# Kernel tuning notes

Measured on AMD Instinct MI355X. Metric: run time of the kernel, lower is better.

## Reference

```python
import jax, jax.numpy as jnp
import numpy as np

D_MODEL = 1024
SEL_DIM = 64
CONFIGS = [(4, 32), (8, 64), (16, 128)]  # (heads, dim)
B, T = 2, 2048


def setup_inputs() -> dict:
    key = jax.random.key(0)
    ks = jax.random.split(key, 20)
    s = 0.02  # init scale for stability
    inp = {
        "x": jax.random.normal(ks[0], (B, T, D_MODEL), jnp.float32),
        "sel_w1": jax.random.normal(ks[1], (SEL_DIM, D_MODEL), jnp.float32) * s,
        "sel_b1": jnp.zeros((SEL_DIM,), jnp.float32),
        "sel_w2": jax.random.normal(ks[2], (SEL_DIM, SEL_DIM), jnp.float32) * s,
        "sel_b2": jnp.zeros((SEL_DIM,), jnp.float32),
        "sel_w3": jax.random.normal(ks[3], (len(CONFIGS), SEL_DIM), jnp.float32) * s,
        "sel_b3": jnp.zeros((len(CONFIGS),), jnp.float32),
    }
    for i, (h, d) in enumerate(CONFIGS):
        inp[f"qw{i}"] = jax.random.normal(ks[4 + 3 * i], (h * d, D_MODEL), jnp.float32) * s
        inp[f"kw{i}"] = jax.random.normal(ks[5 + 3 * i], (d, D_MODEL), jnp.float32) * s
        inp[f"ww{i}"] = jax.random.normal(ks[6 + 3 * i], (h, D_MODEL), jnp.float32) * s
    return inp


def _seq_features(x):
    # x: [b,t,d]
    b, t, d = x.shape
    seq_mean = jnp.mean(x, axis=1, keepdims=True)            # [b,1,d]
    seq_std = jnp.std(x, axis=1, keepdims=True, ddof=1)      # torch.std is unbiased
    pos = (jnp.arange(t, dtype=x.dtype) / t)[None, :, None]  # [1,t,1] broadcast to [b,t,d]
    return x + seq_mean + seq_std + pos * 0.1


def _forward(x, sel_w1, sel_b1, sel_w2, sel_b2, sel_w3, sel_b3,
             qw0, kw0, ww0, qw1, kw1, ww1, qw2, kw2, ww2):
    b, t, dm = x.shape
    feats = _seq_features(x)
    h1 = jax.nn.relu(feats @ sel_w1.T + sel_b1)
    h2 = jax.nn.relu(h1 @ sel_w2.T + sel_b2)
    config_probs = jax.nn.softmax(h2 @ sel_w3.T + sel_b3, axis=-1)  # [b,t,ncfg]

    per_cfg = [(qw0, kw0, ww0), (qw1, kw1, ww1), (qw2, kw2, ww2)]
    final = jnp.zeros((b, t, t), dtype=x.dtype)
    for i, ((heads, dim), (qw, kw, ww)) in enumerate(zip(CONFIGS, per_cfg)):
        q = (x @ qw.T).reshape(b, t, heads, dim)   # [b,t,h,d]
        k = x @ kw.T                               # [b,s,d]
        w = x @ ww.T                               # [b,t,h]
        dots = jnp.einsum('bthd,bsd->bths', q, k)  # [b,t,h,s]
        score = jnp.einsum('bths,bth->bts', jax.nn.relu(dots), w)  # relu*weight, sum heads
        final = final + config_probs[:, :, i:i + 1] * score
    return final


def reference(x, sel_w1, sel_b1, sel_w2, sel_b2, sel_w3, sel_b3,
              qw0, kw0, ww0, qw1, kw1, ww1, qw2, kw2, ww2):
    return _forward(x, sel_w1, sel_b1, sel_w2, sel_b2, sel_w3, sel_b3,
                    qw0, kw0, ww0, qw1, kw1, ww1, qw2, kw2, ww2)
```

## Files before the change

kernel.cpp:

```cpp
#include <hip/hip_runtime.h>
#include <hip/hip_fp16.h>
#include <cstdint>
#include <cstddef>
#include <math.h>

#define B_ 2
#define T_ 2048
#define D_ 1024
#define M_ (B_*T_)

#define QO0 0
#define KO0 128
#define WO0 160
#define QO1 168
#define KO1 680
#define WO1 744
#define QO2 752
#define KO2 2800
#define WO2 2928
#define SELO 2944
#define LDN 3072

typedef float f32x16 __attribute__((ext_vector_type(16)));
typedef short bf16x8 __attribute__((ext_vector_type(8)));
typedef unsigned short u16;

__device__ __forceinline__ u16 f2bf(float f) {
    unsigned int u = __float_as_uint(f);
    unsigned int r = (u + 0x7fffu + ((u >> 16) & 1u)) >> 16;
    return (u16)r;
}
__device__ __forceinline__ float bf2f(u16 b) {
    return __uint_as_float(((unsigned int)b) << 16);
}

__device__ __forceinline__ void gload16(const void* g, void* l) {
    __builtin_amdgcn_global_load_lds(
        (const __attribute__((address_space(1))) unsigned int*)g,
        (__attribute__((address_space(3))) unsigned int*)l,
        16, 0, 0);
}

__device__ __forceinline__ void stage_plane(const u16* src_base, int row_stride, int k0,
                                            int rg, int lane, u16* dst) {
    int rl  = lane >> 2;
    int row = rg * 16 + rl;
    int q   = (lane & 3) ^ (rl & 3) ^ ((rl >> 2) & 3);
    const u16* s = src_base + (size_t)row * row_stride + k0 + q * 8;
    gload16(s, dst + rg * 512);
}

__global__ void prep(const float* __restrict__ x, float* __restrict__ part,
                     float* __restrict__ part2, u16* __restrict__ Xh,
                     const float* __restrict__ qw0, const float* __restrict__ kw0,
                     const float* __restrict__ ww0, const float* __restrict__ qw1,
                     const float* __restrict__ kw1, const float* __restrict__ ww1,
                     const float* __restrict__ qw2, const float* __restrict__ kw2,
                     const float* __restrict__ ww2, const float* __restrict__ w1s,
                     u16* __restrict__ Wh) {
    int bid = blockIdx.x;
    if (bid < 64) {
        int d4 = threadIdx.x * 4;
        int tc = bid & 31;
        int b  = bid >> 5;
        size_t base = (size_t)b * T_ * D_ + (size_t)tc * 64 * D_ + d4;
        float4 s = make_float4(0.f, 0.f, 0.f, 0.f);
        float4 s2 = make_float4(0.f, 0.f, 0.f, 0.f);
#pragma unroll 8
        for (int t = 0; t < 64; ++t) {
            float4 v = *(const float4*)(x + base + (size_t)t * D_);
            s.x += v.x; s.y += v.y; s.z += v.z; s.w += v.w;
            s2.x += v.x * v.x; s2.y += v.y * v.y; s2.z += v.z * v.z; s2.w += v.w * v.w;
            ushort4 h;
            h.x = f2bf(v.x); h.y = f2bf(v.y); h.z = f2bf(v.z); h.w = f2bf(v.w);
            *(ushort4*)(Xh + base + (size_t)t * D_) = h;
        }
        *(float4*)(part  + (size_t)(b * 32 + tc) * D_ + d4) = s;
        *(float4*)(part2 + (size_t)(b * 32 + tc) * D_ + d4) = s2;
    } else {
        int row = bid - 64;
        int col = threadIdx.x * 4;
        const float* src = nullptr;
        if      (row < 128)  src = qw0 + (size_t)row * D_;
        else if (row < 160)  src = kw0 + (size_t)(row - 128) * D_;
        else if (row < 164)  src = ww0 + (size_t)(row - 160) * D_;
        else if (row < 168)  src = nullptr;
        else if (row < 680)  src = qw1 + (size_t)(row - 168) * D_;
        else if (row < 744)  src = kw1 + (size_t)(row - 680) * D_;
        else if (row < 752)  src = ww1 + (size_t)(row - 744) * D_;
        else if (row < 2800) src = qw2 + (size_t)(row - 752) * D_;
        else if (row < 2928) src = kw2 + (size_t)(row - 2800) * D_;
        else if (row < 2944) src = ww2 + (size_t)(row - 2928) * D_;
        else if (row < 3008) src = w1s + (size_t)(row - 2944) * D_;
        float4 v = src ? *(const float4*)(src + col) : make_float4(0.f, 0.f, 0.f, 0.f);
        ushort4 h;
        h.x = f2bf(v.x); h.y = f2bf(v.y); h.z = f2bf(v.z); h.w = f2bf(v.w);
        *(ushort4*)&Wh[(size_t)row * D_ + col] = h;
    }
}

__global__ void stats2(const float* __restrict__ part, const float* __restrict__ part2,
                       const float* __restrict__ w1,
                       float* __restrict__ msd, float* __restrict__ s1) {
    __shared__ float msL[1024];
    __shared__ float ps[64][17];
    __shared__ float pw[64][17];
    int b = blockIdx.x, tid = threadIdx.x;
    float s = 0.f, s2 = 0.f;
#pragma unroll 8
    for (int i = 0; i < 32; ++i) {
        s  += part [(b * 32 + i) * D_ + tid];
        s2 += part2[(b * 32 + i) * D_ + tid];
    }
    float mean = s / (float)T_;
    float var  = (s2 - (float)T_ * mean * mean) / (float)(T_ - 1);
    msL[tid] = mean + sqrtf(fmaxf(var, 0.f));
    __syncthreads();
    int j = tid >> 4, cc = tid & 15;
    float am = 0.f, aw = 0.f;
    const float* wr = w1 + (size_t)j * D_ + cc * 64;
    const float* mr = msL + cc * 64;
    for (int dd = 0; dd < 64; ++dd) { float w = wr[dd]; am += mr[dd] * w; aw += w; }
    ps[j][cc] = am; pw[j][cc] = aw;
    __syncthreads();
    if (tid < 64) {
        float sm = 0.f, sw = 0.f;
        for (int i = 0; i < 16; ++i) { sm += ps[tid][i]; sw += pw[tid][i]; }
        msd[b * 64 + tid] = sm;
        if (b == 0) s1[tid] = sw;
    }
}

__global__ __launch_bounds__(512, 2) void proj_gemm(
    const u16* __restrict__ Xh, const u16* __restrict__ Wh, u16* __restrict__ Ph) {
    __shared__ u16 As[2][16384], Bs[2][16384];
    int tid = threadIdx.x;
    int wave = tid >> 6, lane = tid & 63;
    int wt = wave >> 2, wn = wave & 3;
    int fm = lane & 31, hv = lane >> 5;
    int tkey = (fm & 3) ^ ((fm >> 2) & 3);

    int n = blockIdx.x;
    int p = (n & 7) * 24 + (n >> 3);
    int bm = (p / 12) * 256, bn = (p % 12) * 256;

    const u16* xh = Xh + (size_t)bm * D_;
    const u16* wh = Wh + (size_t)bn * D_;

    f32x16 acc[4][2];
#pragma unroll
    for (int i = 0; i < 4; ++i)
#pragma unroll
        for (int j = 0; j < 2; ++j)
#pragma unroll
            for (int r = 0; r < 16; ++r) acc[i][j][r] = 0.f;

    auto stage = [&](int buf, int k0) {
#pragma unroll
        for (int i = 0; i < 8; ++i) {
            int j = wave * 8 + i;
            int mat = j >> 5;
            int jj  = j & 31;
            int pl  = jj >> 4, rg = jj & 15;
            stage_plane(mat ? wh : xh, D_, k0 + pl * 32, rg, lane,
                        (mat ? Bs[buf] : As[buf]) + pl * 8192);
        }
    };

    stage(0, 0);
    for (int kc = 0; kc < 16; ++kc) {
        int buf = kc & 1;
        if (kc < 15) {
            stage(buf ^ 1, (kc + 1) * 64);
            asm volatile("s_waitcnt vmcnt(8)" ::: "memory");
        } else {
            asm volatile("s_waitcnt vmcnt(0)" ::: "memory");
        }
        __builtin_amdgcn_s_barrier();
        __builtin_amdgcn_sched_barrier(0);

        bf16x8 a[2][4], bq[2][2];
        auto loadks = [&](int ks, int sl) {
            int pl = ks >> 1;
            int slot8 = (((ks & 1) * 2 + hv) ^ tkey) * 8;
#pragma unroll
            for (int ti = 0; ti < 4; ++ti)
                a[sl][ti] = *(const bf16x8*)&As[buf][pl * 8192 + (wt * 128 + ti * 32 + fm) * 32 + slot8];
#pragma unroll
            for (int tj = 0; tj < 2; ++tj)
                bq[sl][tj] = *(const bf16x8*)&Bs[buf][pl * 8192 + (wn * 64 + tj * 32 + fm) * 32 + slot8];
        };
        loadks(0, 0);
#pragma unroll
        for (int ks = 0; ks < 4; ++ks) {
            if (ks < 3) loadks(ks + 1, (ks + 1) & 1);
            int sl = ks & 1;
            __builtin_amdgcn_s_setprio(1);
#pragma unroll
            for (int ti = 0; ti < 4; ++ti)
#pragma unroll
                for (int tj = 0; tj < 2; ++tj)
                    acc[ti][tj] = __builtin_amdgcn_mfma_f32_32x32x16_bf16(
                        a[sl][ti], bq[sl][tj], acc[ti][tj], 0, 0, 0);
            __builtin_amdgcn_s_setprio(0);
        }
        __builtin_amdgcn_sched_barrier(0);
        __builtin_amdgcn_s_barrier();
    }

#pragma unroll
    for (int ti = 0; ti < 4; ++ti)
#pragma unroll
        for (int tj = 0; tj < 2; ++tj)
#pragma unroll
            for (int r = 0; r < 16; ++r) {
                int row = bm + wt * 128 + ti * 32 + (r & 3) + 8 * (r >> 2) + 4 * hv;
                int col = bn + wn * 64 + tj * 32 + fm;
                Ph[(size_t)row * LDN + col] = f2bf(acc[ti][tj][r]);
            }
}

__global__ void selector2(const u16* __restrict__ Ph,
                          const float* __restrict__ msd, const float* __restrict__ s1,
                          const float* __restrict__ b1, const float* __restrict__ w2,
                          const float* __restrict__ b2, const float* __restrict__ w3,
                          const float* __restrict__ b3, __half* __restrict__ WP) {
    __shared__ float h1s[4][64];
    __shared__ float h2s[4][64];
    __shared__ float lg[4][3];
    int tid = threadIdx.x;
    int slot = tid >> 6, j = tid & 63;
    int bt = blockIdx.x * 4 + slot;
    int b = bt >> 11, t = bt & 2047;
    size_t pidx = (size_t)bt * LDN + SELO + j;
    float v = bf2f(Ph[pidx])
            + msd[b * 64 + j] + 0.1f * ((float)t / (float)T_) * s1[j] + b1[j];
    h1s[slot][j] = fmaxf(v, 0.f);
    __syncthreads();
    float a2 = b2[j];
    {
        const float4* w2v = (const float4*)(w2 + (size_t)j * 64);
        const float4* h1v = (const float4*)h1s[slot];
#pragma unroll
        for (int d = 0; d < 16; ++d) {
            float4 wv = w2v[d], hv4 = h1v[d];
            a2 = fmaf(hv4.x, wv.x, a2);
            a2 = fmaf(hv4.y, wv.y, a2);
            a2 = fmaf(hv4.z, wv.z, a2);
            a2 = fmaf(hv4.w, wv.w, a2);
        }
    }
    h2s[slot][j] = fmaxf(a2, 0.f);
    __syncthreads();
    if (j < 3) {
        float a3 = b3[j];
        const float4* w3v = (const float4*)(w3 + (size_t)j * 64);
        const float4* h2v = (const float4*)h2s[slot];
#pragma unroll
        for (int d = 0; d < 16; ++d) {
            float4 wv = w3v[d], hv4 = h2v[d];
            a3 = fmaf(hv4.x, wv.x, a3);
            a3 = fmaf(hv4.y, wv.y, a3);
            a3 = fmaf(hv4.z, wv.z, a3);
            a3 = fmaf(hv4.w, wv.w, a3);
        }
        lg[slot][j] = a3;
    }
    __syncthreads();
    if (j < 28) {
        float m = fmaxf(lg[slot][0], fmaxf(lg[slot][1], lg[slot][2]));
        float e0 = expf(lg[slot][0] - m), e1 = expf(lg[slot][1] - m), e2 = expf(lg[slot][2] - m);
        float inv = 1.f / (e0 + e1 + e2);
        int wcol = (j < 4) ? (WO0 + j) : ((j < 12) ? (WO1 + j - 4) : (WO2 + j - 12));
        float p = ((j < 4) ? e0 : ((j < 12) ? e1 : e2)) * inv;
        float w = bf2f(Ph[(size_t)bt * LDN + wcol]);
        WP[(size_t)(b * 28 + j) * T_ + t] = __float2half(w * p);
    }
}

__device__ __forceinline__ int qcol_of(int c) {
    if (c < 2)  return QO0 + c * 64;
    if (c < 10) return QO1 + (c - 2) * 64;
    return QO2 + (c - 10) * 64;
}

__global__ __launch_bounds__(256, 2) void score_kernel(
    const u16* __restrict__ Ph, const __half* __restrict__ WP, float* __restrict__ out) {
    __shared__ u16 Qs[2][8192];
    __shared__ u16 Ks[4 * 4096];
    __shared__ __half wpL[3584];
    int tid = threadIdx.x;
    int wave = tid >> 6, lane = tid & 63;
    int wt = wave >> 1, wn = wave & 1;
    int fm = lane & 31, hv = lane >> 5;
    int tkey = (fm & 3) ^ ((fm >> 2) & 3);

    int n = blockIdx.z * 256 + blockIdx.y * 16 + blockIdx.x;
    int p = (n & 7) * 4 + (n >> 7);
    int xb = (n >> 3) & 15;
    int b = p >> 4, yb = p & 15;
    int t0 = yb * 128, s0 = xb * 128;

    const u16* Pq = Ph + (size_t)(b * T_ + t0) * LDN;
    const u16* Pk = Ph + (size_t)(b * T_ + s0) * LDN;

    auto stageQ = [&](int buf, int qcol) {
#pragma unroll
        for (int i = 0; i < 4; ++i) {
            int j = (wave << 2) + i;
            int pl = j >> 3, rg = j & 7;
            stage_plane(Pq, LDN, qcol + pl * 32, rg, lane, &Qs[buf][pl * 4096]);
        }
    };

#pragma unroll
    for (int i = 0; i < 6; ++i) {
        int j = i * 4 + wave;
        int pl = j >> 3, rg = j & 7;
        int col = (pl == 0) ? KO0 : ((pl == 1) ? KO1 : KO1 + 32);
        stage_plane(Pk, LDN, col, rg, lane, &Ks[pl * 4096]);
    }
#pragma unroll
    for (int i = 0; i < 2; ++i) {
        int j = i * 4 + wave;
        if (j < 7) {
            const __half* src = WP + (size_t)(b * 28 + j * 4 + (lane >> 4)) * T_ + t0 + (lane & 15) * 8;
            gload16(src, (u16*)wpL + j * 512);
        }
    }
    stageQ(0, QO0);

    f32x16 outacc[2][2], dots[2][2], Z16;
#pragma unroll
    for (int r = 0; r < 16; ++r) Z16[r] = 0.f;
#pragma unroll
    for (int i = 0; i < 2; ++i)
#pragma unroll
        for (int j = 0; j < 2; ++j)
#pragma unroll
            for (int r = 0; r < 16; ++r) { outacc[i][j][r] = 0.f; dots[i][j][r] = 0.f; }

    auto epi = [&](int g) {
#pragma unroll
        for (int ti = 0; ti < 2; ++ti) {
            int rowbase = wt * 64 + ti * 32 + 4 * hv;
#pragma unroll
            for (int rq = 0; rq < 4; ++rq) {
                __half2 wpq[2];
                *(short4*)wpq = *(const short4*)&wpL[g * 128 + rowbase + rq * 8];
                float2 f01 = __half22float2(wpq[0]);
                float2 f23 = __half22float2(wpq[1]);
                float wv[4] = {f01.x, f01.y, f23.x, f23.y};
#pragma unroll
                for (int tj = 0; tj < 2; ++tj)
#pragma unroll
                    for (int r2 = 0; r2 < 4; ++r2) {
                        int r = rq * 4 + r2;
                        outacc[ti][tj][r] += fmaxf(dots[ti][tj][r], 0.f) * wv[r2];
                    }
            }
        }
    };

    auto runPhase = [&](int c, int kpA, int kpB, bool z0, bool midBreak,
                        int gMid, bool hasEnd, int gEnd) {
        if (c + 1 < 42) {
            stageQ((c + 1) & 1, qcol_of(c + 1));
            asm volatile("s_waitcnt vmcnt(4)" ::: "memory");
        } else {
            asm volatile("s_waitcnt vmcnt(0)" ::: "memory");
        }
        __builtin_amdgcn_s_barrier();
        __builtin_amdgcn_sched_barrier(0);
        const u16* qb = Qs[c & 1];

        bf16x8 kf[2][2], qf[2][2];
        auto loadks = [&](int ks, int sl) {
            int kp = (ks < 2) ? kpA : kpB;
            int slot8 = (((ks & 1) * 2 + hv) ^ tkey) * 8;
#pragma unroll
            for (int tj = 0; tj < 2; ++tj)
                kf[sl][tj] = *(const bf16x8*)&Ks[kp * 4096 + (wn * 64 + tj * 32 + fm) * 32 + slot8];
#pragma unroll
            for (int ti = 0; ti < 2; ++ti)
                qf[sl][ti] = *(const bf16x8*)&qb[(ks >> 1) * 4096 + (wt * 64 + ti * 32 + fm) * 32 + slot8];
        };
        loadks(0, 0);
#pragma unroll
        for (int ks = 0; ks < 4; ++ks) {
            if (ks < 3) loadks(ks + 1, (ks + 1) & 1);
            bool zero = (ks == 0 && z0) || (ks == 2 && midBreak);
            int sl = ks & 1;
            __builtin_amdgcn_s_setprio(1);
#pragma unroll
            for (int ti = 0; ti < 2; ++ti)
#pragma unroll
                for (int tj = 0; tj < 2; ++tj)
                    dots[ti][tj] = __builtin_amdgcn_mfma_f32_32x32x16_bf16(
                        qf[sl][ti], kf[sl][tj], zero ? Z16 : dots[ti][tj], 0, 0, 0);
            __builtin_amdgcn_s_setprio(0);
            if (ks == 1 && midBreak) epi(gMid);
            if (ks == 3 && hasEnd)   epi(gEnd);
        }
        __builtin_amdgcn_sched_barrier(0);
        __builtin_amdgcn_s_barrier();
    };

#pragma unroll
    for (int c = 0; c < 2; ++c)
        runPhase(c, 0, 0, true, true, 2 * c, true, 2 * c + 1);
    for (int h = 0; h < 8; ++h) {
        runPhase(2 + h, 1, 2, true, false, -1, true, 4 + h);
        if (h == 7) {
            for (int j = wave; j < 32; j += 4) {
                int pl = j >> 3, rg = j & 7;
                stage_plane(Pk, LDN, KO2 + pl * 32, rg, lane, &Ks[pl * 4096]);
            }
        }
    }
    for (int h = 0; h < 16; ++h) {
        runPhase(10 + 2 * h, 0, 1, true, false, -1, false, -1);
        runPhase(11 + 2 * h, 2, 3, false, false, -1, true, 12 + h);
    }

#pragma unroll
    for (int ti = 0; ti < 2; ++ti)
#pragma unroll
        for (int tj = 0; tj < 2; ++tj)
#pragma unroll
            for (int r = 0; r < 16; ++r) {
                int trow = wt * 64 + ti * 32 + (r & 3) + 8 * (r >> 2) + 4 * hv;
                int scol = wn * 64 + tj * 32 + fm;
                __builtin_nontemporal_store(outacc[ti][tj][r],
                    &out[(size_t)(b * T_ + t0 + trow) * T_ + (s0 + scol)]);
            }
}

extern "C" void kernel_launch(void* const* d_in, const int* in_sizes, int n_in,
                              void* d_out, int out_size, void* d_ws, size_t ws_size,
                              hipStream_t stream) {
    const float* x   = (const float*)d_in[0];
    const float* w1  = (const float*)d_in[1];
    const float* b1  = (const float*)d_in[2];
    const float* w2  = (const float*)d_in[3];
    const float* b2  = (const float*)d_in[4];
    const float* w3  = (const float*)d_in[5];
    const float* b3  = (const float*)d_in[6];
    const float* qw0 = (const float*)d_in[7];
    const float* kw0 = (const float*)d_in[8];
    const float* ww0 = (const float*)d_in[9];
    const float* qw1 = (const float*)d_in[10];
    const float* kw1 = (const float*)d_in[11];
    const float* ww1 = (const float*)d_in[12];
    const float* qw2 = (const float*)d_in[13];
    const float* kw2 = (const float*)d_in[14];
    const float* ww2 = (const float*)d_in[15];
    float* out = (float*)d_out;

    float* fb = (float*)d_ws;
    float* PA  = fb; fb += (size_t)B_ * 32 * D_;
    float* PA2 = fb; fb += (size_t)B_ * 32 * D_;
    float* MSD = fb; fb += 128;
    float* S1  = fb; fb += 64;
    __half* WP = (__half*)fb; fb += (size_t)B_ * 28 * T_ / 2;
    u16* ub = (u16*)fb;
    u16* Wh = ub; ub += (size_t)LDN * D_;
    u16* Xh = ub; ub += (size_t)M_ * D_;
    u16* Ph = ub; ub += (size_t)M_ * LDN;

    prep<<<dim3(64 + LDN), 256, 0, stream>>>(x, PA, PA2, Xh,
                                             qw0, kw0, ww0, qw1, kw1, ww1,
                                             qw2, kw2, ww2, w1, Wh);
    stats2<<<dim3(B_), 1024, 0, stream>>>(PA, PA2, w1, MSD, S1);
    proj_gemm<<<dim3(192), 512, 0, stream>>>(Xh, Wh, Ph);
    selector2<<<dim3(M_ / 4), 256, 0, stream>>>(Ph, MSD, S1, b1, w2, b2, w3, b3, WP);
    score_kernel<<<dim3(T_ / 128, T_ / 128, B_), 256, 0, stream>>>(Ph, WP, out);
}
```

Baseline: 255.1 us.

## Fuse stats into proj_gemm extra blocks and selector MLP into score kernel

The stats reduction kernel now runs as two extra blocks appended to the projection GEMM grid. The selector MLP and softmax are recomputed inside each score block for its 128 query rows, writing weighted probabilities straight to shared memory. This removes two kernel launches and the global WP buffer round trip. In exchange, each score block does the selector MLP redundantly (16x across s-tiles) with serial per-row shuffle reductions before its main loop.

```diff
diff --git a/kernel.cpp b/kernel.cpp
--- a/kernel.cpp
+++ b/kernel.cpp
@@ -99,42 +99,49 @@
     }
 }
 
-__global__ void stats2(const float* __restrict__ part, const float* __restrict__ part2,
-                       const float* __restrict__ w1,
-                       float* __restrict__ msd, float* __restrict__ s1) {
-    __shared__ float msL[1024];
-    __shared__ float ps[64][17];
-    __shared__ float pw[64][17];
-    int b = blockIdx.x, tid = threadIdx.x;
-    float s = 0.f, s2 = 0.f;
-#pragma unroll 8
-    for (int i = 0; i < 32; ++i) {
-        s  += part [(b * 32 + i) * D_ + tid];
-        s2 += part2[(b * 32 + i) * D_ + tid];
-    }
-    float mean = s / (float)T_;
-    float var  = (s2 - (float)T_ * mean * mean) / (float)(T_ - 1);
-    msL[tid] = mean + sqrtf(fmaxf(var, 0.f));
-    __syncthreads();
-    int j = tid >> 4, cc = tid & 15;
-    float am = 0.f, aw = 0.f;
-    const float* wr = w1 + (size_t)j * D_ + cc * 64;
-    const float* mr = msL + cc * 64;
-    for (int dd = 0; dd < 64; ++dd) { float w = wr[dd]; am += mr[dd] * w; aw += w; }
-    ps[j][cc] = am; pw[j][cc] = aw;
-    __syncthreads();
-    if (tid < 64) {
-        float sm = 0.f, sw = 0.f;
-        for (int i = 0; i < 16; ++i) { sm += ps[tid][i]; sw += pw[tid][i]; }
-        msd[b * 64 + tid] = sm;
-        if (b == 0) s1[tid] = sw;
-    }
-}
-
 __global__ __launch_bounds__(512, 2) void proj_gemm(
-    const u16* __restrict__ Xh, const u16* __restrict__ Wh, u16* __restrict__ Ph) {
+    const u16* __restrict__ Xh, const u16* __restrict__ Wh, u16* __restrict__ Ph,
+    const float* __restrict__ part, const float* __restrict__ part2,
+    const float* __restrict__ w1, float* __restrict__ msd, float* __restrict__ s1) {
     __shared__ u16 As[2][16384], Bs[2][16384];
     int tid = threadIdx.x;
+
+    if (blockIdx.x >= 192) {
+        int b = blockIdx.x - 192;
+        float* msL = (float*)&As[0][0];
+        float* psp = msL + 1024;
+        float* pwp = psp + 64 * 9;
+#pragma unroll
+        for (int half = 0; half < 2; ++half) {
+            int c = tid + half * 512;
+            float s = 0.f, s2 = 0.f;
+#pragma unroll 8
+            for (int i = 0; i < 32; ++i) {
+                s  += part [(b * 32 + i) * D_ + c];
+                s2 += part2[(b * 32 + i) * D_ + c];
+            }
+            float mean = s / (float)T_;
+            float var  = (s2 - (float)T_ * mean * mean) / (float)(T_ - 1);
+            msL[c] = mean + sqrtf(fmaxf(var, 0.f));
+        }
+        __syncthreads();
+        int j = tid >> 3, cc = tid & 7;
+        float am = 0.f, aw = 0.f;
+        const float* wr = w1 + (size_t)j * D_ + cc * 128;
+        const float* mr = msL + cc * 128;
+        for (int dd = 0; dd < 128; ++dd) { float w = wr[dd]; am += mr[dd] * w; aw += w; }
+        psp[j * 9 + cc] = am; pwp[j * 9 + cc] = aw;
+        __syncthreads();
+        if (tid < 64) {
+            float sm = 0.f, sw = 0.f;
+#pragma unroll
+            for (int i = 0; i < 8; ++i) { sm += psp[tid * 9 + i]; sw += pwp[tid * 9 + i]; }
+            msd[b * 64 + tid] = sm;
+            if (b == 0) s1[tid] = sw;
+        }
+        return;
+    }
+
     int wave = tid >> 6, lane = tid & 63;
     int wt = wave >> 2, wn = wave & 3;
     int fm = lane & 31, hv = lane >> 5;
@@ -220,64 +227,6 @@
             }
 }
 
-__global__ void selector2(const u16* __restrict__ Ph,
-                          const float* __restrict__ msd, const float* __restrict__ s1,
-                          const float* __restrict__ b1, const float* __restrict__ w2,
-                          const float* __restrict__ b2, const float* __restrict__ w3,
-                          const float* __restrict__ b3, __half* __restrict__ WP) {
-    __shared__ float h1s[4][64];
-    __shared__ float h2s[4][64];
-    __shared__ float lg[4][3];
-    int tid = threadIdx.x;
-    int slot = tid >> 6, j = tid & 63;
-    int bt = blockIdx.x * 4 + slot;
-    int b = bt >> 11, t = bt & 2047;
-    size_t pidx = (size_t)bt * LDN + SELO + j;
-    float v = bf2f(Ph[pidx])
-            + msd[b * 64 + j] + 0.1f * ((float)t / (float)T_) * s1[j] + b1[j];
-    h1s[slot][j] = fmaxf(v, 0.f);
-    __syncthreads();
-    float a2 = b2[j];
-    {
-        const float4* w2v = (const float4*)(w2 + (size_t)j * 64);
-        const float4* h1v = (const float4*)h1s[slot];
-#pragma unroll
-        for (int d = 0; d < 16; ++d) {
-            float4 wv = w2v[d], hv4 = h1v[d];
-            a2 = fmaf(hv4.x, wv.x, a2);
-            a2 = fmaf(hv4.y, wv.y, a2);
-            a2 = fmaf(hv4.z, wv.z, a2);
-            a2 = fmaf(hv4.w, wv.w, a2);
-        }
-    }
-    h2s[slot][j] = fmaxf(a2, 0.f);
-    __syncthreads();
-    if (j < 3) {
-        float a3 = b3[j];
-        const float4* w3v = (const float4*)(w3 + (size_t)j * 64);
-        const float4* h2v = (const float4*)h2s[slot];
-#pragma unroll
-        for (int d = 0; d < 16; ++d) {
-            float4 wv = w3v[d], hv4 = h2v[d];
-            a3 = fmaf(hv4.x, wv.x, a3);
-            a3 = fmaf(hv4.y, wv.y, a3);
-            a3 = fmaf(hv4.z, wv.z, a3);
-            a3 = fmaf(hv4.w, wv.w, a3);
-        }
-        lg[slot][j] = a3;
-    }
-    __syncthreads();
-    if (j < 28) {
-        float m = fmaxf(lg[slot][0], fmaxf(lg[slot][1], lg[slot][2]));
-        float e0 = expf(lg[slot][0] - m), e1 = expf(lg[slot][1] - m), e2 = expf(lg[slot][2] - m);
-        float inv = 1.f / (e0 + e1 + e2);
-        int wcol = (j < 4) ? (WO0 + j) : ((j < 12) ? (WO1 + j - 4) : (WO2 + j - 12));
-        float p = ((j < 4) ? e0 : ((j < 12) ? e1 : e2)) * inv;
-        float w = bf2f(Ph[(size_t)bt * LDN + wcol]);
-        WP[(size_t)(b * 28 + j) * T_ + t] = __float2half(w * p);
-    }
-}
-
 __device__ __forceinline__ int qcol_of(int c) {
     if (c < 2)  return QO0 + c * 64;
     if (c < 10) return QO1 + (c - 2) * 64;
@@ -285,10 +234,15 @@
 }
 
 __global__ __launch_bounds__(256, 2) void score_kernel(
-    const u16* __restrict__ Ph, const __half* __restrict__ WP, float* __restrict__ out) {
+    const u16* __restrict__ Ph, const float* __restrict__ msd,
+    const float* __restrict__ s1, const float* __restrict__ b1,
+    const float* __restrict__ w2, const float* __restrict__ b2,
+    const float* __restrict__ w3, const float* __restrict__ b3,
+    float* __restrict__ out) {
     __shared__ u16 Qs[2][8192];
     __shared__ u16 Ks[4 * 4096];
     __shared__ __half wpL[3584];
+    __shared__ __align__(16) float h1s[4][64];
     int tid = threadIdx.x;
     int wave = tid >> 6, lane = tid & 63;
     int wt = wave >> 1, wn = wave & 1;
@@ -320,15 +274,57 @@
         int col = (pl == 0) ? KO0 : ((pl == 1) ? KO1 : KO1 + 32);
         stage_plane(Pk, LDN, col, rg, lane, &Ks[pl * 4096]);
     }
-#pragma unroll
-    for (int i = 0; i < 2; ++i) {
-        int j = i * 4 + wave;
-        if (j < 7) {
-            const __half* src = WP + (size_t)(b * 28 + j * 4 + (lane >> 4)) * T_ + t0 + (lane & 15) * 8;
-            gload16(src, (u16*)wpL + j * 512);
-        }
-    }
     stageQ(0, QO0);
+
+    {
+        int j = lane;
+        float msdv = msd[b * 64 + j];
+        float s1v  = s1[j];
+        float b1v  = b1[j];
+        float b2v  = b2[j];
+        float w30 = w3[0 * 64 + j], w31 = w3[1 * 64 + j], w32 = w3[2 * 64 + j];
+        float b30 = b3[0], b31 = b3[1], b32v = b3[2];
+        float* h1p = &h1s[wave][0];
+        const float4* w2v = (const float4*)(w2 + (size_t)j * 64);
+        for (int it = 0; it < 32; ++it) {
+            int row = wave * 32 + it;
+            float selv = bf2f(Pq[(size_t)row * LDN + SELO + j]);
+            float tpos = (float)(t0 + row) / (float)T_;
+            float h1 = fmaxf(selv + msdv + 0.1f * tpos * s1v + b1v, 0.f);
+            h1p[j] = h1;
+            asm volatile("s_waitcnt lgkmcnt(0)" ::: "memory");
+            __builtin_amdgcn_sched_barrier(0);
+            float a2 = b2v;
+            const float4* hvp = (const float4*)h1p;
+#pragma unroll
+            for (int d = 0; d < 16; ++d) {
+                float4 wv = w2v[d], h4 = hvp[d];
+                a2 = fmaf(h4.x, wv.x, a2);
+                a2 = fmaf(h4.y, wv.y, a2);
+                a2 = fmaf(h4.z, wv.z, a2);
+                a2 = fmaf(h4.w, wv.w, a2);
+            }
+            float h2 = fmaxf(a2, 0.f);
+            float p0 = h2 * w30, p1 = h2 * w31, p2 = h2 * w32;
+#pragma unroll
+            for (int off = 32; off; off >>= 1) {
+                p0 += __shfl_xor(p0, off);
+                p1 += __shfl_xor(p1, off);
+                p2 += __shfl_xor(p2, off);
+            }
+            p0 += b30; p1 += b31; p2 += b32v;
+            float m = fmaxf(p0, fmaxf(p1, p2));
+            float e0 = expf(p0 - m), e1 = expf(p1 - m), e2 = expf(p2 - m);
+            float inv = 1.f / (e0 + e1 + e2);
+            if (j < 28) {
+                int wcol = (j < 4) ? (WO0 + j) : ((j < 12) ? (WO1 + j - 4) : (WO2 + j - 12));
+                float pg = ((j < 4) ? e0 : ((j < 12) ? e1 : e2)) * inv;
+                float w = bf2f(Pq[(size_t)row * LDN + wcol]);
+                wpL[j * 128 + row] = __float2half(w * pg);
+            }
+        }
+    }
+    asm volatile("s_waitcnt lgkmcnt(0)" ::: "memory");
 
     f32x16 outacc[2][2], dots[2][2], Z16;
 #pragma unroll
@@ -462,7 +458,6 @@
     float* PA2 = fb; fb += (size_t)B_ * 32 * D_;
     float* MSD = fb; fb += 128;
     float* S1  = fb; fb += 64;
-    __half* WP = (__half*)fb; fb += (size_t)B_ * 28 * T_ / 2;
     u16* ub = (u16*)fb;
     u16* Wh = ub; ub += (size_t)LDN * D_;
     u16* Xh = ub; ub += (size_t)M_ * D_;
@@ -471,8 +466,7 @@
     prep<<<dim3(64 + LDN), 256, 0, stream>>>(x, PA, PA2, Xh,
                                              qw0, kw0, ww0, qw1, kw1, ww1,
                                              qw2, kw2, ww2, w1, Wh);
-    stats2<<<dim3(B_), 1024, 0, stream>>>(PA, PA2, w1, MSD, S1);
-    proj_gemm<<<dim3(192), 512, 0, stream>>>(Xh, Wh, Ph);
-    selector2<<<dim3(M_ / 4), 256, 0, stream>>>(Ph, MSD, S1, b1, w2, b2, w3, b3, WP);
-    score_kernel<<<dim3(T_ / 128, T_ / 128, B_), 256, 0, stream>>>(Ph, WP, out);
-}
+    proj_gemm<<<dim3(194), 512, 0, stream>>>(Xh, Wh, Ph, PA, PA2, w1, MSD, S1);
+    score_kernel<<<dim3(T_ / 128, T_ / 128, B_), 256, 0, stream>>>(
+        Ph, MSD, S1, b1, w2, b2, w3, b3, out);
+}
```

After: 347.7 us. +36.3%, slower.
